# Performance work log

Measured on AMD Instinct MI355X. Metric: run time of the kernel, lower is better.

Reference implementation:

```python
import jax, jax.numpy as jnp
import numpy as np

K, D = 512, 64
B, H, W = 32, 64, 64


def setup_inputs() -> dict:
    key = jax.random.key(0)
    k1, k2 = jax.random.split(key)
    z_e_x = jax.random.normal(k1, (B, D, H, W), dtype=jnp.float32)
    # nn.Embedding weight initialized uniform(-1/K, 1/K)
    codebook = jax.random.uniform(k2, (K, D), dtype=jnp.float32,
                                  minval=-1.0 / K, maxval=1.0 / K)
    return {"z_e_x": z_e_x, "codebook": codebook}


def _quantize_indices(flat, codebook):
    # distances[n,k] = ||c_k||^2 + ||x_n||^2 - 2 x_n . c_k  (addmm form)
    cb_sqr = jnp.sum(codebook * codebook, axis=1)            # [K]
    x_sqr = jnp.sum(flat * flat, axis=1, keepdims=True)      # [N,1]
    distances = cb_sqr + x_sqr - 2.0 * (flat @ codebook.T)   # [N,K]
    return jnp.argmin(distances, axis=1)                     # [N]


def reference(z_e_x, codebook):
    # VQEmbedding.straight_through forward: returns (z_q_x, z_q_x_bar), both NCHW.
    b, d, h, w = z_e_x.shape
    x = jnp.transpose(z_e_x, (0, 2, 3, 1))       # NHWC
    flat = x.reshape(-1, d)                      # [N,D]
    idx = _quantize_indices(flat, codebook)      # [N]
    codes = jnp.take(codebook, idx, axis=0).reshape(b, h, w, d)
    z_q = jnp.transpose(codes, (0, 3, 1, 2))     # NCHW
    # z_q_x (detached codebook path) and z_q_x_bar (live codebook path) are
    # numerically identical in the forward pass.
    return (z_q, z_q)
```

## Files before the change

kernel.cpp:

```cpp
#include <hip/hip_runtime.h>


typedef short bf16x8 __attribute__((ext_vector_type(8)));
typedef float f32x4  __attribute__((ext_vector_type(4)));

#define KCODES 512
#define DDIM 64
#define HWSZ 4096
#define NPOS 131072
#define POSB 128
#define NBLK (NPOS / POSB)
#define OUT2_OFF 8388608
#define S_X 132
#define S_X4 (S_X / 4)

__device__ __forceinline__ unsigned short f2bf_rne(float f) {
    unsigned u = __builtin_bit_cast(unsigned, f);
    unsigned r = u + 0x7FFFu + ((u >> 16) & 1u);
    return (unsigned short)(r >> 16);
}
__device__ __forceinline__ float bf2f(unsigned short h) {
    unsigned u = ((unsigned)h) << 16;
    return __builtin_bit_cast(float, u);
}

__device__ __forceinline__ float np_sumsq64(const float* __restrict__ a) {
#pragma clang fp contract(off)
    float r0 = a[0]*a[0], r1 = a[1]*a[1], r2 = a[2]*a[2], r3 = a[3]*a[3];
    float r4 = a[4]*a[4], r5 = a[5]*a[5], r6 = a[6]*a[6], r7 = a[7]*a[7];
#pragma unroll
    for (int i = 8; i < 64; i += 8) {
        r0 += a[i+0]*a[i+0]; r1 += a[i+1]*a[i+1];
        r2 += a[i+2]*a[i+2]; r3 += a[i+3]*a[i+3];
        r4 += a[i+4]*a[i+4]; r5 += a[i+5]*a[i+5];
        r6 += a[i+6]*a[i+6]; r7 += a[i+7]*a[i+7];
    }
    return ((r0+r1)+(r2+r3)) + ((r4+r5)+(r6+r7));
}

__global__ __launch_bounds__(256) void vq_prep(
    const float* __restrict__ cb, unsigned short* __restrict__ wsb,
    float* __restrict__ wscb)
{
    if (blockIdx.x < 128) {
        int u = blockIdx.x * 256 + threadIdx.x;
        int k = u >> 6, d = u & 63;
        float c = cb[u];
        unsigned short ch = f2bf_rne(c);
        float clf = c - bf2f(ch);
        unsigned short cl = f2bf_rne(clf);
        int tile = k >> 4, n = k & 15;
        int chunk = d >> 5, quad = (d >> 3) & 3, j = d & 7;
        int lane = quad * 16 + n;
        size_t base = ((((size_t)tile*2 + chunk)*2 + 0)*64 + lane)*8 + j;
        wsb[base]       = (unsigned short)ch;
        wsb[base + 512] = (unsigned short)cl;
    } else {
        int k = (blockIdx.x - 128) * 256 + threadIdx.x;
        if (k < KCODES) wscb[k] = np_sumsq64(cb + k * DDIM);
    }
}

__global__ __launch_bounds__(256, 4) void vq_main(
    const float* __restrict__ z, const float* __restrict__ cb,
    const unsigned short* __restrict__ wsb, const float* __restrict__ wscb,
    float* __restrict__ out)
{
#pragma clang fp contract(off)
    __shared__ float4 s_xbuf4[DDIM * S_X4];
    __shared__ float s_cbsqr[KCODES];
    __shared__ float s_xsqr[POSB];
    __shared__ float s_part[2 * POSB];
    __shared__ int   s_idx[POSB];
    __shared__ int   s_flist[POSB];
    __shared__ int   s_cnt;
    float* s_regA = (float*)s_xbuf4;

    const int tid = threadIdx.x;
    const int wv = tid >> 6, ln = tid & 63;
    const int m = ln & 15, q = ln >> 4;
    const int n0 = blockIdx.x * POSB;
    const long gbase = (long)(n0 >> 12) * (DDIM * HWSZ) + (n0 & 4095);

    if (tid == 0) s_cnt = 0;
    s_cbsqr[tid] = wscb[tid];
    s_cbsqr[tid + 256] = wscb[tid + 256];

    {
        const float4* z4 = (const float4*)(z + gbase);
#pragma unroll
        for (int i = 0; i < 8; ++i) {
            int v = i * 256 + tid;
            int d = v >> 5, p4 = v & 31;
            s_xbuf4[d * S_X4 + p4] = z4[d * (HWSZ / 4) + p4];
        }
    }
    __syncthreads();

    {
        int p = tid & 127, h = tid >> 7;
        float r0 = 0.f, r1 = 0.f, r2 = 0.f, r3 = 0.f;
#pragma unroll
        for (int i = 0; i < 8; ++i) {
            float a0 = s_regA[(8*i + 4*h + 0) * S_X + p];
            float a1 = s_regA[(8*i + 4*h + 1) * S_X + p];
            float a2 = s_regA[(8*i + 4*h + 2) * S_X + p];
            float a3 = s_regA[(8*i + 4*h + 3) * S_X + p];
            r0 += a0*a0; r1 += a1*a1; r2 += a2*a2; r3 += a3*a3;
        }
        s_part[h * POSB + p] = (r0 + r1) + (r2 + r3);
    }

    bf16x8 Ah[4], Al[4];
#pragma unroll
    for (int rt = 0; rt < 2; ++rt)
#pragma unroll
        for (int c = 0; c < 2; ++c) {
            int pos = wv * 32 + rt * 16 + m;
            bf16x8 ah, al;
#pragma unroll
            for (int j = 0; j < 8; ++j) {
                float xv = s_regA[(c*32 + q*8 + j) * S_X + pos];
                unsigned short hh = f2bf_rne(xv);
                float lo = xv - bf2f(hh);
                ah[j] = (short)hh;
                al[j] = (short)f2bf_rne(lo);
            }
            Ah[rt*2 + c] = ah; Al[rt*2 + c] = al;
        }
    __syncthreads();
    if (tid < POSB) s_xsqr[tid] = s_part[tid] + s_part[POSB + tid];
    __syncthreads();

    float m1[8], m2[8]; int t1[8];
#pragma unroll
    for (int i = 0; i < 8; ++i) { m1[i] = 3.4e38f; m2[i] = 3.4e38f; t1[i] = 0; }

    {
        const unsigned short* wbl = wsb + ln * 8;
#pragma unroll 2
        for (int t = 0; t < 32; ++t) {
            const unsigned short* nb = wbl + t * 2048;
            bf16x8 Bh0 = *(const bf16x8*)(nb + 0);
            bf16x8 Bl0 = *(const bf16x8*)(nb + 512);
            bf16x8 Bh1 = *(const bf16x8*)(nb + 1024);
            bf16x8 Bl1 = *(const bf16x8*)(nb + 1536);
            float cbv = s_cbsqr[t * 16 + m];
#pragma unroll
            for (int rt = 0; rt < 2; ++rt) {
                f32x4 acc = {0.f, 0.f, 0.f, 0.f};
                acc = __builtin_amdgcn_mfma_f32_16x16x32_bf16(Al[rt*2+0], Bh0, acc, 0,0,0);
                acc = __builtin_amdgcn_mfma_f32_16x16x32_bf16(Ah[rt*2+0], Bl0, acc, 0,0,0);
                acc = __builtin_amdgcn_mfma_f32_16x16x32_bf16(Ah[rt*2+0], Bh0, acc, 0,0,0);
                acc = __builtin_amdgcn_mfma_f32_16x16x32_bf16(Al[rt*2+1], Bh1, acc, 0,0,0);
                acc = __builtin_amdgcn_mfma_f32_16x16x32_bf16(Ah[rt*2+1], Bl1, acc, 0,0,0);
                acc = __builtin_amdgcn_mfma_f32_16x16x32_bf16(Ah[rt*2+1], Bh1, acc, 0,0,0);
#pragma unroll
                for (int r = 0; r < 4; ++r) {
                    float sc = fmaf(-2.f, acc[r], cbv);
                    int cell = rt * 4 + r;
                    bool lt = sc < m1[cell];
                    m2[cell] = fminf(m2[cell], lt ? m1[cell] : sc);
                    if (lt) { m1[cell] = sc; t1[cell] = t; }
                }
            }
        }
    }

#pragma unroll
    for (int cell = 0; cell < 8; ++cell) {
        int rt = cell >> 2, r = cell & 3;
        float v1 = m1[cell], v2 = m2[cell];
        int i1 = t1[cell] * 16 + m;
#pragma unroll
        for (int s = 1; s < 16; s <<= 1) {
            float o1 = __shfl_xor(v1, s);
            float o2 = __shfl_xor(v2, s);
            int   oi = __shfl_xor(i1, s);
            bool take = (o1 < v1) || (o1 == v1 && oi < i1);
            float lose = take ? v1 : o1;
            if (take) { v1 = o1; i1 = oi; }
            v2 = fminf(fminf(v2, o2), lose);
        }
        if (m == 0) {
            int pos = wv * 32 + rt * 16 + q * 4 + r;
            float xs = s_xsqr[pos];
            float sx = 8.0f * sqrtf(xs) * 1.01f;
            float amax = 0.00196f * sx + 0.01f;
            float eps = 1.5f * (3.0f * 1.52587890625e-5f * 0.00196f * sx
                                + 500.f * 5.96e-8f * amax);
            float delta = 2.4e-7f * (xs + 1.0f) + 64.f * 1.2e-7f * amax;
            float W = 2.f * eps + 2.f * delta + 1e-9f;
            int flag = (v2 - v1 <= W) ? (1 << 30) : 0;
            s_idx[pos] = i1 | flag;
        }
    }
    __syncthreads();
    if (tid < POSB) {
        if (s_idx[tid] & (1 << 30)) {
            int slot = atomicAdd(&s_cnt, 1);
            s_flist[slot] = tid;
        }
    }
    __syncthreads();

    const int cnt = s_cnt;
    for (int i = wv; i < cnt; i += 4) {
        int p = __builtin_amdgcn_readfirstlane(s_flist[i]);
        float xv = s_regA[ln * S_X + p];
        float xs = s_xsqr[p];
        float dot[8];
#pragma unroll
        for (int j = 0; j < 8; ++j) dot[j] = 0.f;
        const float* crow = cb + (ln * 8) * DDIM;
        for (int dc = 0; dc < 16; ++dc) {
            float x0 = __shfl(xv, dc*4 + 0);
            float x1 = __shfl(xv, dc*4 + 1);
            float x2 = __shfl(xv, dc*4 + 2);
            float x3 = __shfl(xv, dc*4 + 3);
#pragma unroll
            for (int j = 0; j < 8; ++j) {
                float4 cv = *(const float4*)(crow + j * DDIM + dc * 4);
                dot[j] = fmaf(x0, cv.x, dot[j]);
                dot[j] = fmaf(x1, cv.y, dot[j]);
                dot[j] = fmaf(x2, cv.z, dot[j]);
                dot[j] = fmaf(x3, cv.w, dot[j]);
            }
        }
        float bv = 3.4e38f; int bi = 0;
#pragma unroll
        for (int j = 0; j < 8; ++j) {
            int k = ln * 8 + j;
            float tt = s_cbsqr[k] + xs;
            float e = fmaf(-2.f, dot[j], tt);
            if (e < bv) { bv = e; bi = k; }
        }
#pragma unroll
        for (int s = 1; s < 64; s <<= 1) {
            float ov = __shfl_xor(bv, s); int oi = __shfl_xor(bi, s);
            if (ov < bv || (ov == bv && oi < bi)) { bv = ov; bi = oi; }
        }
        if (ln == 0) s_idx[p] = bi;
    }
    __syncthreads();

    {
        int p = tid & 127, hf = tid >> 7;
        int idx = s_idx[p] & 0x3FFFFFFF;
        const float4* crow4 = (const float4*)(cb + idx * DDIM + hf * 32);
#pragma unroll
        for (int j4 = 0; j4 < 8; ++j4) {
            float4 cv = crow4[j4];
            int d = hf * 32 + j4 * 4;
            s_regA[(d + 0) * S_X + p] = cv.x;
            s_regA[(d + 1) * S_X + p] = cv.y;
            s_regA[(d + 2) * S_X + p] = cv.z;
            s_regA[(d + 3) * S_X + p] = cv.w;
        }
    }
    __syncthreads();

    {
        float4* o4 = (float4*)(out + gbase);
#pragma unroll
        for (int i = 0; i < 8; ++i) {
            int v = i * 256 + tid;
            int d = v >> 5, p4 = v & 31;
            float4 val = s_xbuf4[d * S_X4 + p4];
            size_t off = (size_t)d * (HWSZ / 4) + p4;
            o4[off] = val;
            o4[off + (OUT2_OFF / 4)] = val;
        }
    }
}

extern "C" void kernel_launch(void* const* d_in, const int* in_sizes, int n_in,
                              void* d_out, int out_size, void* d_ws, size_t ws_size,
                              hipStream_t stream) {
    const float* z  = (const float*)d_in[0];
    const float* cb = (const float*)d_in[1];
    float* out = (float*)d_out;
    unsigned short* wsb = (unsigned short*)d_ws;
    float* wscb = (float*)((char*)d_ws + 131072);
    vq_prep<<<130, 256, 0, stream>>>(cb, wsb, wscb);
    vq_main<<<NBLK, 256, 0, stream>>>(z, cb, wsb, wscb, out);
}
```

Before: 150.1 us.

## Make per-wave shared tiles and drop block barriers before the distance loop

Each wave now loads its own 32 positions into a private shared-memory slice, computes the squared norms with a lane shuffle, and handles its own ambiguous positions through a wave ballot instead of a block-wide atomic list. This removes three block barriers and the shared codebook-norm copy, which is now read straight from global memory. The cost is that ambiguous-position refinement is no longer spread over all four waves, so one wave can carry more of it, and the codebook-norm reads go through global memory. The final gather reuses the same buffer under a different stride.

New measurement: 177.7 us. +18.4%, slower.

```diff
diff --git a/kernel.cpp b/kernel.cpp
--- a/kernel.cpp
+++ b/kernel.cpp
@@ -11,8 +11,8 @@
 #define POSB 128
 #define NBLK (NPOS / POSB)
 #define OUT2_OFF 8388608
-#define S_X 132
-#define S_X4 (S_X / 4)
+#define XW 34
+#define CW 132
 
 __device__ __forceinline__ unsigned short f2bf_rne(float f) {
     unsigned u = __builtin_bit_cast(unsigned, f);
@@ -67,14 +67,9 @@
     float* __restrict__ out)
 {
 #pragma clang fp contract(off)
-    __shared__ float4 s_xbuf4[DDIM * S_X4];
-    __shared__ float s_cbsqr[KCODES];
+    __shared__ __align__(16) float s_x[4 * DDIM * XW];
     __shared__ float s_xsqr[POSB];
-    __shared__ float s_part[2 * POSB];
     __shared__ int   s_idx[POSB];
-    __shared__ int   s_flist[POSB];
-    __shared__ int   s_cnt;
-    float* s_regA = (float*)s_xbuf4;
 
     const int tid = threadIdx.x;
     const int wv = tid >> 6, ln = tid & 63;
@@ -82,33 +77,38 @@
     const int n0 = blockIdx.x * POSB;
     const long gbase = (long)(n0 >> 12) * (DDIM * HWSZ) + (n0 & 4095);
 
-    if (tid == 0) s_cnt = 0;
-    s_cbsqr[tid] = wscb[tid];
-    s_cbsqr[tid + 256] = wscb[tid + 256];
-
-    {
-        const float4* z4 = (const float4*)(z + gbase);
-#pragma unroll
-        for (int i = 0; i < 8; ++i) {
-            int v = i * 256 + tid;
-            int d = v >> 5, p4 = v & 31;
-            s_xbuf4[d * S_X4 + p4] = z4[d * (HWSZ / 4) + p4];
-        }
-    }
-    __syncthreads();
-
-    {
-        int p = tid & 127, h = tid >> 7;
+    float* xw = s_x + wv * (DDIM * XW);
+
+    {
+        const float* zw = z + gbase + wv * 32;
+        float4 v4[8];
+#pragma unroll
+        for (int i = 0; i < 8; ++i) {
+            int d = i * 8 + (ln >> 3), c4 = (ln & 7) * 4;
+            v4[i] = *(const float4*)(zw + (long)d * HWSZ + c4);
+        }
+#pragma unroll
+        for (int i = 0; i < 8; ++i) {
+            int d = i * 8 + (ln >> 3), c4 = (ln & 7) * 4;
+            *(float2*)(xw + d * XW + c4)     = make_float2(v4[i].x, v4[i].y);
+            *(float2*)(xw + d * XW + c4 + 2) = make_float2(v4[i].z, v4[i].w);
+        }
+    }
+
+    {
+        int pl = ln >> 1, h = ln & 1;
         float r0 = 0.f, r1 = 0.f, r2 = 0.f, r3 = 0.f;
 #pragma unroll
         for (int i = 0; i < 8; ++i) {
-            float a0 = s_regA[(8*i + 4*h + 0) * S_X + p];
-            float a1 = s_regA[(8*i + 4*h + 1) * S_X + p];
-            float a2 = s_regA[(8*i + 4*h + 2) * S_X + p];
-            float a3 = s_regA[(8*i + 4*h + 3) * S_X + p];
+            float a0 = xw[(8*i + 4*h + 0) * XW + pl];
+            float a1 = xw[(8*i + 4*h + 1) * XW + pl];
+            float a2 = xw[(8*i + 4*h + 2) * XW + pl];
+            float a3 = xw[(8*i + 4*h + 3) * XW + pl];
             r0 += a0*a0; r1 += a1*a1; r2 += a2*a2; r3 += a3*a3;
         }
-        s_part[h * POSB + p] = (r0 + r1) + (r2 + r3);
+        float part = (r0 + r1) + (r2 + r3);
+        float other = __shfl_xor(part, 1);
+        if (h == 0) s_xsqr[wv * 32 + pl] = part + other;
     }
 
     bf16x8 Ah[4], Al[4];
@@ -116,11 +116,11 @@
     for (int rt = 0; rt < 2; ++rt)
 #pragma unroll
         for (int c = 0; c < 2; ++c) {
-            int pos = wv * 32 + rt * 16 + m;
+            int col = rt * 16 + m;
             bf16x8 ah, al;
 #pragma unroll
             for (int j = 0; j < 8; ++j) {
-                float xv = s_regA[(c*32 + q*8 + j) * S_X + pos];
+                float xv = xw[(c*32 + q*8 + j) * XW + col];
                 unsigned short hh = f2bf_rne(xv);
                 float lo = xv - bf2f(hh);
                 ah[j] = (short)hh;
@@ -128,9 +128,6 @@
             }
             Ah[rt*2 + c] = ah; Al[rt*2 + c] = al;
         }
-    __syncthreads();
-    if (tid < POSB) s_xsqr[tid] = s_part[tid] + s_part[POSB + tid];
-    __syncthreads();
 
     float m1[8], m2[8]; int t1[8];
 #pragma unroll
@@ -145,7 +142,7 @@
             bf16x8 Bl0 = *(const bf16x8*)(nb + 512);
             bf16x8 Bh1 = *(const bf16x8*)(nb + 1024);
             bf16x8 Bl1 = *(const bf16x8*)(nb + 1536);
-            float cbv = s_cbsqr[t * 16 + m];
+            float cbv = wscb[t * 16 + m];
 #pragma unroll
             for (int rt = 0; rt < 2; ++rt) {
                 f32x4 acc = {0.f, 0.f, 0.f, 0.f};
@@ -195,52 +192,48 @@
             s_idx[pos] = i1 | flag;
         }
     }
-    __syncthreads();
-    if (tid < POSB) {
-        if (s_idx[tid] & (1 << 30)) {
-            int slot = atomicAdd(&s_cnt, 1);
-            s_flist[slot] = tid;
-        }
-    }
-    __syncthreads();
-
-    const int cnt = s_cnt;
-    for (int i = wv; i < cnt; i += 4) {
-        int p = __builtin_amdgcn_readfirstlane(s_flist[i]);
-        float xv = s_regA[ln * S_X + p];
-        float xs = s_xsqr[p];
-        float dot[8];
-#pragma unroll
-        for (int j = 0; j < 8; ++j) dot[j] = 0.f;
-        const float* crow = cb + (ln * 8) * DDIM;
-        for (int dc = 0; dc < 16; ++dc) {
-            float x0 = __shfl(xv, dc*4 + 0);
-            float x1 = __shfl(xv, dc*4 + 1);
-            float x2 = __shfl(xv, dc*4 + 2);
-            float x3 = __shfl(xv, dc*4 + 3);
+
+    {
+        int myidx = s_idx[wv * 32 + (ln & 31)];
+        unsigned long long fm = __ballot((ln < 32) && (myidx & (1 << 30)));
+        while (fm) {
+            int pl = __builtin_ctzll(fm);
+            fm &= fm - 1;
+            float xv = xw[ln * XW + pl];
+            float xs = s_xsqr[wv * 32 + pl];
+            float dot[8];
+#pragma unroll
+            for (int j = 0; j < 8; ++j) dot[j] = 0.f;
+            const float* crow = cb + (ln * 8) * DDIM;
+            for (int dc = 0; dc < 16; ++dc) {
+                float x0 = __shfl(xv, dc*4 + 0);
+                float x1 = __shfl(xv, dc*4 + 1);
+                float x2 = __shfl(xv, dc*4 + 2);
+                float x3 = __shfl(xv, dc*4 + 3);
+#pragma unroll
+                for (int j = 0; j < 8; ++j) {
+                    float4 cv = *(const float4*)(crow + j * DDIM + dc * 4);
+                    dot[j] = fmaf(x0, cv.x, dot[j]);
+                    dot[j] = fmaf(x1, cv.y, dot[j]);
+                    dot[j] = fmaf(x2, cv.z, dot[j]);
+                    dot[j] = fmaf(x3, cv.w, dot[j]);
+                }
+            }
+            float bv = 3.4e38f; int bi = 0;
 #pragma unroll
             for (int j = 0; j < 8; ++j) {
-                float4 cv = *(const float4*)(crow + j * DDIM + dc * 4);
-                dot[j] = fmaf(x0, cv.x, dot[j]);
-                dot[j] = fmaf(x1, cv.y, dot[j]);
-                dot[j] = fmaf(x2, cv.z, dot[j]);
-                dot[j] = fmaf(x3, cv.w, dot[j]);
-            }
-        }
-        float bv = 3.4e38f; int bi = 0;
-#pragma unroll
-        for (int j = 0; j < 8; ++j) {
-            int k = ln * 8 + j;
-            float tt = s_cbsqr[k] + xs;
-            float e = fmaf(-2.f, dot[j], tt);
-            if (e < bv) { bv = e; bi = k; }
-        }
-#pragma unroll
-        for (int s = 1; s < 64; s <<= 1) {
-            float ov = __shfl_xor(bv, s); int oi = __shfl_xor(bi, s);
-            if (ov < bv || (ov == bv && oi < bi)) { bv = ov; bi = oi; }
-        }
-        if (ln == 0) s_idx[p] = bi;
+                int k = ln * 8 + j;
+                float tt = wscb[k] + xs;
+                float e = fmaf(-2.f, dot[j], tt);
+                if (e < bv) { bv = e; bi = k; }
+            }
+#pragma unroll
+            for (int s = 1; s < 64; s <<= 1) {
+                float ov = __shfl_xor(bv, s); int oi = __shfl_xor(bi, s);
+                if (ov < bv || (ov == bv && oi < bi)) { bv = ov; bi = oi; }
+            }
+            if (ln == 0) s_idx[wv * 32 + pl] = bi;
+        }
     }
     __syncthreads();
 
@@ -252,21 +245,22 @@
         for (int j4 = 0; j4 < 8; ++j4) {
             float4 cv = crow4[j4];
             int d = hf * 32 + j4 * 4;
-            s_regA[(d + 0) * S_X + p] = cv.x;
-            s_regA[(d + 1) * S_X + p] = cv.y;
-            s_regA[(d + 2) * S_X + p] = cv.z;
-            s_regA[(d + 3) * S_X + p] = cv.w;
+            s_x[(d + 0) * CW + p] = cv.x;
+            s_x[(d + 1) * CW + p] = cv.y;
+            s_x[(d + 2) * CW + p] = cv.z;
+            s_x[(d + 3) * CW + p] = cv.w;
         }
     }
     __syncthreads();
 
     {
         float4* o4 = (float4*)(out + gbase);
+        const float4* c4 = (const float4*)s_x;
 #pragma unroll
         for (int i = 0; i < 8; ++i) {
             int v = i * 256 + tid;
             int d = v >> 5, p4 = v & 31;
-            float4 val = s_xbuf4[d * S_X4 + p4];
+            float4 val = c4[d * (CW / 4) + p4];
             size_t off = (size_t)d * (HWSZ / 4) + p4;
             o4[off] = val;
             o4[off + (OUT2_OFF / 4)] = val;
```

## Split VQ kernel into index-screening and codebook-scatter kernels

Applied to the files above, without the earlier changes.

Splits the fused kernel in two. The first kernel computes the argmin indices and writes them temporarily into the output buffer. A second kernel reads those indices back, gathers the codebook rows through shared memory, and writes both NCHW outputs. This may lower register and LDS pressure in each kernel, but it costs an extra launch and a global round-trip for the indices.

Result: slower. 182.6 us (+21.6%).

```diff
diff --git a/kernel.cpp b/kernel.cpp
--- a/kernel.cpp
+++ b/kernel.cpp
@@ -61,7 +61,7 @@
     }
 }
 
-__global__ __launch_bounds__(256, 4) void vq_main(
+__global__ __launch_bounds__(256, 4) void vq_screen(
     const float* __restrict__ z, const float* __restrict__ cb,
     const unsigned short* __restrict__ wsb, const float* __restrict__ wscb,
     float* __restrict__ out)
@@ -244,29 +244,47 @@
     }
     __syncthreads();
 
+    if (tid < POSB)
+        ((int*)out)[gbase + tid] = s_idx[tid] & 0x3FFFFFFF;
+}
+
+__global__ __launch_bounds__(256, 4) void vq_scatter(
+    const float* __restrict__ cb, float* __restrict__ out)
+{
+    __shared__ float s_codes[DDIM * S_X];
+    __shared__ int   s_pidx[POSB];
+
+    const int tid = threadIdx.x;
+    const int n0 = blockIdx.x * POSB;
+    const long gbase = (long)(n0 >> 12) * (DDIM * HWSZ) + (n0 & 4095);
+
+    if (tid < POSB) s_pidx[tid] = ((const int*)out)[gbase + tid];
+    __syncthreads();
+
     {
         int p = tid & 127, hf = tid >> 7;
-        int idx = s_idx[p] & 0x3FFFFFFF;
+        int idx = s_pidx[p];
         const float4* crow4 = (const float4*)(cb + idx * DDIM + hf * 32);
 #pragma unroll
         for (int j4 = 0; j4 < 8; ++j4) {
             float4 cv = crow4[j4];
             int d = hf * 32 + j4 * 4;
-            s_regA[(d + 0) * S_X + p] = cv.x;
-            s_regA[(d + 1) * S_X + p] = cv.y;
-            s_regA[(d + 2) * S_X + p] = cv.z;
-            s_regA[(d + 3) * S_X + p] = cv.w;
+            s_codes[(d + 0) * S_X + p] = cv.x;
+            s_codes[(d + 1) * S_X + p] = cv.y;
+            s_codes[(d + 2) * S_X + p] = cv.z;
+            s_codes[(d + 3) * S_X + p] = cv.w;
         }
     }
     __syncthreads();
 
     {
         float4* o4 = (float4*)(out + gbase);
+        const float4* c4 = (const float4*)s_codes;
 #pragma unroll
         for (int i = 0; i < 8; ++i) {
             int v = i * 256 + tid;
             int d = v >> 5, p4 = v & 31;
-            float4 val = s_xbuf4[d * S_X4 + p4];
+            float4 val = c4[d * S_X4 + p4];
             size_t off = (size_t)d * (HWSZ / 4) + p4;
             o4[off] = val;
             o4[off + (OUT2_OFF / 4)] = val;
@@ -283,5 +301,6 @@
     unsigned short* wsb = (unsigned short*)d_ws;
     float* wscb = (float*)((char*)d_ws + 131072);
     vq_prep<<<130, 256, 0, stream>>>(cb, wsb, wscb);
-    vq_main<<<NBLK, 256, 0, stream>>>(z, cb, wsb, wscb, out);
-}
+    vq_screen<<<NBLK, 256, 0, stream>>>(z, cb, wsb, wscb, out);
+    vq_scatter<<<NBLK, 256, 0, stream>>>(cb, out);
+}
```

## Stage codebook tiles into LDS with double-buffered async global-to-LDS loads

Applied to the files above, without the earlier changes.

Before, each wave read the bf16 hi/lo codebook fragments straight from global memory on every iteration. Now groups of 4 code tiles are prefetched into a double-buffered LDS staging area, reusing the s_regA space, via global_load_lds. The next group's load overlaps the MFMA work on the current group. Because s_regA is overwritten, the fallback exact path now rereads x from global memory. This adds one block barrier per group and LDS read traffic.

Measured after the change: 151.2 us. No clear change (+0.8%).

```diff
diff --git a/kernel.cpp b/kernel.cpp
--- a/kernel.cpp
+++ b/kernel.cpp
@@ -13,6 +13,11 @@
 #define OUT2_OFF 8388608
 #define S_X 132
 #define S_X4 (S_X / 4)
+
+#define GLD_LDS16(gsrc, ldst)                                                   \
+    __builtin_amdgcn_global_load_lds(                                           \
+        (const __attribute__((address_space(1))) void*)(gsrc),                  \
+        (__attribute__((address_space(3))) void*)(ldst), 16, 0, 0)
 
 __device__ __forceinline__ unsigned short f2bf_rne(float f) {
     unsigned u = __builtin_bit_cast(unsigned, f);
@@ -129,7 +134,17 @@
             Ah[rt*2 + c] = ah; Al[rt*2 + c] = al;
         }
     __syncthreads();
+
+    char* const stg0 = (char*)s_regA;
+    char* const stg1 = (char*)s_regA + 16384;
+    {
+        const unsigned short* src = wsb + (0 * 4 + wv) * 2048 + ln * 8;
+        char* dst = stg0 + wv * 4096;
+#pragma unroll
+        for (int i = 0; i < 4; ++i) GLD_LDS16(src + i * 512, dst + i * 1024);
+    }
     if (tid < POSB) s_xsqr[tid] = s_part[tid] + s_part[POSB + tid];
+    asm volatile("s_waitcnt vmcnt(0)" ::: "memory");
     __syncthreads();
 
     float m1[8], m2[8]; int t1[8];
@@ -137,33 +152,47 @@
     for (int i = 0; i < 8; ++i) { m1[i] = 3.4e38f; m2[i] = 3.4e38f; t1[i] = 0; }
 
     {
-        const unsigned short* wbl = wsb + ln * 8;
-#pragma unroll 2
-        for (int t = 0; t < 32; ++t) {
-            const unsigned short* nb = wbl + t * 2048;
-            bf16x8 Bh0 = *(const bf16x8*)(nb + 0);
-            bf16x8 Bl0 = *(const bf16x8*)(nb + 512);
-            bf16x8 Bh1 = *(const bf16x8*)(nb + 1024);
-            bf16x8 Bl1 = *(const bf16x8*)(nb + 1536);
-            float cbv = s_cbsqr[t * 16 + m];
-#pragma unroll
-            for (int rt = 0; rt < 2; ++rt) {
-                f32x4 acc = {0.f, 0.f, 0.f, 0.f};
-                acc = __builtin_amdgcn_mfma_f32_16x16x32_bf16(Al[rt*2+0], Bh0, acc, 0,0,0);
-                acc = __builtin_amdgcn_mfma_f32_16x16x32_bf16(Ah[rt*2+0], Bl0, acc, 0,0,0);
-                acc = __builtin_amdgcn_mfma_f32_16x16x32_bf16(Ah[rt*2+0], Bh0, acc, 0,0,0);
-                acc = __builtin_amdgcn_mfma_f32_16x16x32_bf16(Al[rt*2+1], Bh1, acc, 0,0,0);
-                acc = __builtin_amdgcn_mfma_f32_16x16x32_bf16(Ah[rt*2+1], Bl1, acc, 0,0,0);
-                acc = __builtin_amdgcn_mfma_f32_16x16x32_bf16(Ah[rt*2+1], Bh1, acc, 0,0,0);
-#pragma unroll
-                for (int r = 0; r < 4; ++r) {
-                    float sc = fmaf(-2.f, acc[r], cbv);
-                    int cell = rt * 4 + r;
-                    bool lt = sc < m1[cell];
-                    m2[cell] = fminf(m2[cell], lt ? m1[cell] : sc);
-                    if (lt) { m1[cell] = sc; t1[cell] = t; }
+        char* cur = stg0;
+        char* nxt = stg1;
+        for (int g = 0; g < 8; ++g) {
+            if (g < 7) {
+                const unsigned short* src = wsb + ((g + 1) * 4 + wv) * 2048 + ln * 8;
+                char* dst = nxt + wv * 4096;
+#pragma unroll
+                for (int i = 0; i < 4; ++i) GLD_LDS16(src + i * 512, dst + i * 1024);
+            }
+            const unsigned short* sb = (const unsigned short*)cur;
+#pragma unroll
+            for (int ti = 0; ti < 4; ++ti) {
+                int t = g * 4 + ti;
+                const unsigned short* s = sb + ti * 2048 + ln * 8;
+                bf16x8 Bh0 = *(const bf16x8*)(s);
+                bf16x8 Bl0 = *(const bf16x8*)(s + 512);
+                bf16x8 Bh1 = *(const bf16x8*)(s + 1024);
+                bf16x8 Bl1 = *(const bf16x8*)(s + 1536);
+                float cbv = s_cbsqr[t * 16 + m];
+#pragma unroll
+                for (int rt = 0; rt < 2; ++rt) {
+                    f32x4 acc = {0.f, 0.f, 0.f, 0.f};
+                    acc = __builtin_amdgcn_mfma_f32_16x16x32_bf16(Al[rt*2+0], Bh0, acc, 0,0,0);
+                    acc = __builtin_amdgcn_mfma_f32_16x16x32_bf16(Ah[rt*2+0], Bl0, acc, 0,0,0);
+                    acc = __builtin_amdgcn_mfma_f32_16x16x32_bf16(Ah[rt*2+0], Bh0, acc, 0,0,0);
+                    acc = __builtin_amdgcn_mfma_f32_16x16x32_bf16(Al[rt*2+1], Bh1, acc, 0,0,0);
+                    acc = __builtin_amdgcn_mfma_f32_16x16x32_bf16(Ah[rt*2+1], Bl1, acc, 0,0,0);
+                    acc = __builtin_amdgcn_mfma_f32_16x16x32_bf16(Ah[rt*2+1], Bh1, acc, 0,0,0);
+#pragma unroll
+                    for (int r = 0; r < 4; ++r) {
+                        float sc = fmaf(-2.f, acc[r], cbv);
+                        int cell = rt * 4 + r;
+                        bool lt = sc < m1[cell];
+                        m2[cell] = fminf(m2[cell], lt ? m1[cell] : sc);
+                        if (lt) { m1[cell] = sc; t1[cell] = t; }
+                    }
                 }
             }
+            asm volatile("s_waitcnt vmcnt(0)" ::: "memory");
+            __syncthreads();
+            char* tmp = cur; cur = nxt; nxt = tmp;
         }
     }
 
@@ -207,7 +236,7 @@
     const int cnt = s_cnt;
     for (int i = wv; i < cnt; i += 4) {
         int p = __builtin_amdgcn_readfirstlane(s_flist[i]);
-        float xv = s_regA[ln * S_X + p];
+        float xv = z[gbase + (long)ln * HWSZ + p];
         float xs = s_xsqr[p];
         float dot[8];
 #pragma unroll
```
